# Performance work log

Measured on AMD Instinct MI355X. Metric: run time of the kernel, lower is better.

The kernel has to match this reference:

```python
import jax, jax.numpy as jnp
import numpy as np

NUM_CODES = 512
CODE_DIM = 64
COMMITMENT_COST = 0.25


def setup_inputs() -> dict:
    key = jax.random.key(0)
    k1, k2 = jax.random.split(key)
    latents = jax.random.normal(k1, (32, 4096, CODE_DIM), dtype=jnp.float32)
    # nn.Embedding weight init: uniform(-1/num_codes, 1/num_codes)
    codebook = jax.random.uniform(
        k2, (NUM_CODES, CODE_DIM), dtype=jnp.float32,
        minval=-1.0 / NUM_CODES, maxval=1.0 / NUM_CODES)
    return {"latents": latents, "codebook": codebook}


def reference(latents, codebook):
    shape = latents.shape
    flat = latents.reshape(-1, CODE_DIM)                      # [N, D]
    x2 = jnp.sum(flat * flat, axis=-1, keepdims=True)         # [N, 1]
    c2 = jnp.sum(codebook * codebook, axis=-1)                # [K]
    xc = flat @ codebook.T                                    # [N, K] dense GEMM
    dist2 = x2 - 2.0 * xc + c2[None, :]
    codes = jnp.argmin(dist2, axis=-1)                        # [N] int
    quantized = codebook[codes].reshape(shape)                # gather + reshape
    sg = jax.lax.stop_gradient
    commitment_loss = jnp.mean((latents - sg(quantized)) ** 2)
    embedding_loss = jnp.mean((quantized - sg(latents)) ** 2)
    vq_loss = embedding_loss + COMMITMENT_COST * commitment_loss
    quantized_st = latents + sg(quantized - latents)          # straight-through
    return quantized_st, codes.reshape(shape[:-1]), vq_loss
```

## Files before the change

### kernel.cpp

```cpp
#include <hip/hip_runtime.h>

#define NUM_CODES 512
#define CODE_DIM 64
#define N_ROWS (32 * 4096)
#define ROWS_PER_BLOCK 64
#define WAVES_PER_BLOCK 4
#define CODES_PER_WAVE (NUM_CODES / WAVES_PER_BLOCK)
#define KU 4

__global__ void vq_precompute_c2(const float* __restrict__ cb,
                                 float* __restrict__ c2) {
    int k = blockIdx.x * blockDim.x + threadIdx.x;
    if (k < NUM_CODES) {
        const float* c = cb + (size_t)k * CODE_DIM;
        float s = 0.f;
#pragma unroll
        for (int d = 0; d < CODE_DIM; ++d) s = fmaf(c[d], c[d], s);
        c2[k] = s;
    }
}

__global__ __launch_bounds__(256) void vq_main(
    const float* __restrict__ latents, const float* __restrict__ cb,
    const float* __restrict__ c2, float* __restrict__ out_q,
    float* __restrict__ out_codes, float* __restrict__ loss_accum) {
    const int lane = threadIdx.x & 63;
    const int wave = threadIdx.x >> 6;
    const int row = blockIdx.x * ROWS_PER_BLOCK + lane;
    const int chunk0 = __builtin_amdgcn_readfirstlane(wave) * CODES_PER_WAVE;

    const float* __restrict__ x = latents + (size_t)row * CODE_DIM;

    float xv[CODE_DIM];
#pragma unroll
    for (int i = 0; i < CODE_DIM / 4; ++i) {
        float4 v = reinterpret_cast<const float4*>(x)[i];
        xv[4 * i + 0] = v.x;
        xv[4 * i + 1] = v.y;
        xv[4 * i + 2] = v.z;
        xv[4 * i + 3] = v.w;
    }

    float x2 = 0.f;
#pragma unroll
    for (int d = 0; d < CODE_DIM; ++d) x2 = fmaf(xv[d], xv[d], x2);

    float bestd = __builtin_inff();
    int bk = 0;
    for (int kk = 0; kk < CODES_PER_WAVE; kk += KU) {
        const int k0 = chunk0 + kk;
        const float* __restrict__ c = cb + (size_t)k0 * CODE_DIM;
        float s0 = 0.f, s1 = 0.f, s2 = 0.f, s3 = 0.f;
#pragma unroll
        for (int d = 0; d < CODE_DIM; ++d) {
            s0 = fmaf(xv[d], c[d + 0 * CODE_DIM], s0);
            s1 = fmaf(xv[d], c[d + 1 * CODE_DIM], s1);
            s2 = fmaf(xv[d], c[d + 2 * CODE_DIM], s2);
            s3 = fmaf(xv[d], c[d + 3 * CODE_DIM], s3);
        }
        float d0 = (x2 - 2.0f * s0) + c2[k0 + 0];
        float d1 = (x2 - 2.0f * s1) + c2[k0 + 1];
        float d2 = (x2 - 2.0f * s2) + c2[k0 + 2];
        float d3 = (x2 - 2.0f * s3) + c2[k0 + 3];
        if (d0 < bestd) { bestd = d0; bk = k0 + 0; }
        if (d1 < bestd) { bestd = d1; bk = k0 + 1; }
        if (d2 < bestd) { bestd = d2; bk = k0 + 2; }
        if (d3 < bestd) { bestd = d3; bk = k0 + 3; }
    }

    __shared__ float sdist[WAVES_PER_BLOCK][ROWS_PER_BLOCK];
    __shared__ int sidx[WAVES_PER_BLOCK][ROWS_PER_BLOCK];
    sdist[wave][lane] = bestd;
    sidx[wave][lane] = bk;
    __syncthreads();
    if (wave != 0) return;

    float bd = sdist[0][lane];
    int bi = sidx[0][lane];
#pragma unroll
    for (int w = 1; w < WAVES_PER_BLOCK; ++w) {
        float d = sdist[w][lane];
        int i = sidx[w][lane];
        if (d < bd) { bd = d; bi = i; }
    }

    const float* __restrict__ q = cb + (size_t)bi * CODE_DIM;
    float4* oq = reinterpret_cast<float4*>(out_q + (size_t)row * CODE_DIM);
    float lsum = 0.f;
#pragma unroll
    for (int i = 0; i < CODE_DIM / 4; ++i) {
        float4 qq = reinterpret_cast<const float4*>(q)[i];
        float xx0 = xv[4 * i + 0], xx1 = xv[4 * i + 1];
        float xx2 = xv[4 * i + 2], xx3 = xv[4 * i + 3];
        float e0 = xx0 - qq.x, e1 = xx1 - qq.y, e2 = xx2 - qq.z, e3 = xx3 - qq.w;
        lsum = fmaf(e0, e0, lsum);
        lsum = fmaf(e1, e1, lsum);
        lsum = fmaf(e2, e2, lsum);
        lsum = fmaf(e3, e3, lsum);
        float4 ov;
        ov.x = xx0 + (qq.x - xx0);
        ov.y = xx1 + (qq.y - xx1);
        ov.z = xx2 + (qq.z - xx2);
        ov.w = xx3 + (qq.w - xx3);
        oq[i] = ov;
    }
    out_codes[row] = (float)bi;

#pragma unroll
    for (int off = 32; off > 0; off >>= 1) lsum += __shfl_down(lsum, off);
    if (lane == 0) atomicAdd(loss_accum, lsum);
}

__global__ void vq_finalize(const float* __restrict__ acc,
                            float* __restrict__ out_loss) {
    *out_loss = 1.25f * (*acc) / (float)(N_ROWS * CODE_DIM);
}

extern "C" void kernel_launch(void* const* d_in, const int* in_sizes, int n_in,
                              void* d_out, int out_size, void* d_ws, size_t ws_size,
                              hipStream_t stream) {
    const float* latents = (const float*)d_in[0];
    const float* cb      = (const float*)d_in[1];

    float* out_q     = (float*)d_out;
    float* out_codes = out_q + (size_t)N_ROWS * CODE_DIM;
    float* out_loss  = out_codes + N_ROWS;

    float* c2  = (float*)d_ws;
    float* acc = c2 + NUM_CODES;

    hipMemsetAsync(acc, 0, sizeof(float), stream);
    vq_precompute_c2<<<2, 256, 0, stream>>>(cb, c2);
    vq_main<<<N_ROWS / ROWS_PER_BLOCK, 256, 0, stream>>>(latents, cb, c2, out_q,
                                                         out_codes, acc);
    vq_finalize<<<1, 1, 0, stream>>>(acc, out_loss);
}
```

Before: 243.2 us.

## Load codebook rows via scalar SMEM loads and coalesce output epilogue across waves

The distance loop now loads each wave-uniform codebook row and its norm with inline-asm s_load_dwordx16 into SGPRs. This replaces per-lane vector loads of uniform data and lets the FMAs take scalar operands. The epilogue is restructured so all four waves write the quantized output row-by-row, one coalesced dword per lane, instead of wave 0 doing strided per-thread float4 stores. The loss is reduced in shared memory before a single atomic per block. The trade-offs are a full lgkmcnt(0) wait every code with no unrolling, which limits latency hiding, and the latents being re-read from global memory.

```diff
diff --git a/kernel.cpp b/kernel.cpp
--- a/kernel.cpp
+++ b/kernel.cpp
@@ -6,7 +6,15 @@
 #define ROWS_PER_BLOCK 64
 #define WAVES_PER_BLOCK 4
 #define CODES_PER_WAVE (NUM_CODES / WAVES_PER_BLOCK)
-#define KU 4
+
+typedef float f32x16 __attribute__((ext_vector_type(16)));
+
+static __device__ inline const float* uniform_ptr(const float* p) {
+    uint64_t u = (uint64_t)p;
+    uint32_t lo = __builtin_amdgcn_readfirstlane((uint32_t)u);
+    uint32_t hi = __builtin_amdgcn_readfirstlane((uint32_t)(u >> 32));
+    return (const float*)(((uint64_t)hi << 32) | lo);
+}
 
 __global__ void vq_precompute_c2(const float* __restrict__ cb,
                                  float* __restrict__ c2) {
@@ -20,17 +28,16 @@
     }
 }
 
-__global__ __launch_bounds__(256) void vq_main(
+__global__ __launch_bounds__(256, 4) void vq_main(
     const float* __restrict__ latents, const float* __restrict__ cb,
-    const float* __restrict__ c2, float* __restrict__ out_q,
+    const float* __restrict__ c2g, float* __restrict__ out_q,
     float* __restrict__ out_codes, float* __restrict__ loss_accum) {
     const int lane = threadIdx.x & 63;
     const int wave = threadIdx.x >> 6;
     const int row = blockIdx.x * ROWS_PER_BLOCK + lane;
-    const int chunk0 = __builtin_amdgcn_readfirstlane(wave) * CODES_PER_WAVE;
+    const int chunk0 = wave * CODES_PER_WAVE;
 
     const float* __restrict__ x = latents + (size_t)row * CODE_DIM;
-
     float xv[CODE_DIM];
 #pragma unroll
     for (int i = 0; i < CODE_DIM / 4; ++i) {
@@ -40,75 +47,82 @@
         xv[4 * i + 2] = v.z;
         xv[4 * i + 3] = v.w;
     }
-
     float x2 = 0.f;
 #pragma unroll
     for (int d = 0; d < CODE_DIM; ++d) x2 = fmaf(xv[d], xv[d], x2);
 
     float bestd = __builtin_inff();
     int bk = 0;
-    for (int kk = 0; kk < CODES_PER_WAVE; kk += KU) {
-        const int k0 = chunk0 + kk;
-        const float* __restrict__ c = cb + (size_t)k0 * CODE_DIM;
-        float s0 = 0.f, s1 = 0.f, s2 = 0.f, s3 = 0.f;
+    const float* cp = uniform_ptr(cb + (size_t)chunk0 * CODE_DIM);
+    const float* zp = uniform_ptr(c2g + chunk0);
+
+#pragma unroll 1
+    for (int k = 0; k < CODES_PER_WAVE; ++k) {
+        f32x16 c0, c1, c2, c3;
+        float zz;
+        asm volatile("s_load_dwordx16 %0, %1, 0x00" : "=s"(c0) : "s"(cp));
+        asm volatile("s_load_dwordx16 %0, %1, 0x40" : "=s"(c1) : "s"(cp));
+        asm volatile("s_load_dwordx16 %0, %1, 0x80" : "=s"(c2) : "s"(cp));
+        asm volatile("s_load_dwordx16 %0, %1, 0xc0" : "=s"(c3) : "s"(cp));
+        asm volatile("s_load_dword %0, %1, 0x00" : "=s"(zz) : "s"(zp));
+        asm volatile("s_waitcnt lgkmcnt(0)"
+                     : "+s"(c0), "+s"(c1), "+s"(c2), "+s"(c3), "+s"(zz));
+
+        float s = 0.f;
 #pragma unroll
-        for (int d = 0; d < CODE_DIM; ++d) {
-            s0 = fmaf(xv[d], c[d + 0 * CODE_DIM], s0);
-            s1 = fmaf(xv[d], c[d + 1 * CODE_DIM], s1);
-            s2 = fmaf(xv[d], c[d + 2 * CODE_DIM], s2);
-            s3 = fmaf(xv[d], c[d + 3 * CODE_DIM], s3);
-        }
-        float d0 = (x2 - 2.0f * s0) + c2[k0 + 0];
-        float d1 = (x2 - 2.0f * s1) + c2[k0 + 1];
-        float d2 = (x2 - 2.0f * s2) + c2[k0 + 2];
-        float d3 = (x2 - 2.0f * s3) + c2[k0 + 3];
-        if (d0 < bestd) { bestd = d0; bk = k0 + 0; }
-        if (d1 < bestd) { bestd = d1; bk = k0 + 1; }
-        if (d2 < bestd) { bestd = d2; bk = k0 + 2; }
-        if (d3 < bestd) { bestd = d3; bk = k0 + 3; }
+        for (int q = 0; q < 16; ++q) s = fmaf(xv[q], c0[q], s);
+#pragma unroll
+        for (int q = 0; q < 16; ++q) s = fmaf(xv[16 + q], c1[q], s);
+#pragma unroll
+        for (int q = 0; q < 16; ++q) s = fmaf(xv[32 + q], c2[q], s);
+#pragma unroll
+        for (int q = 0; q < 16; ++q) s = fmaf(xv[48 + q], c3[q], s);
+
+        float dist = (x2 - 2.0f * s) + zz;
+        if (dist < bestd) { bestd = dist; bk = chunk0 + k; }
+        cp += CODE_DIM;
+        zp += 1;
     }
 
     __shared__ float sdist[WAVES_PER_BLOCK][ROWS_PER_BLOCK];
     __shared__ int sidx[WAVES_PER_BLOCK][ROWS_PER_BLOCK];
+    __shared__ int sbi[ROWS_PER_BLOCK];
     sdist[wave][lane] = bestd;
     sidx[wave][lane] = bk;
     __syncthreads();
-    if (wave != 0) return;
+    if (wave == 0) {
+        float bd = sdist[0][lane];
+        int bi = sidx[0][lane];
+#pragma unroll
+        for (int w = 1; w < WAVES_PER_BLOCK; ++w) {
+            float d = sdist[w][lane];
+            int i = sidx[w][lane];
+            if (d < bd) { bd = d; bi = i; }
+        }
+        sbi[lane] = bi;
+    }
+    __syncthreads();
 
-    float bd = sdist[0][lane];
-    int bi = sidx[0][lane];
-#pragma unroll
-    for (int w = 1; w < WAVES_PER_BLOCK; ++w) {
-        float d = sdist[w][lane];
-        int i = sidx[w][lane];
-        if (d < bd) { bd = d; bi = i; }
-    }
-
-    const float* __restrict__ q = cb + (size_t)bi * CODE_DIM;
-    float4* oq = reinterpret_cast<float4*>(out_q + (size_t)row * CODE_DIM);
     float lsum = 0.f;
 #pragma unroll
-    for (int i = 0; i < CODE_DIM / 4; ++i) {
-        float4 qq = reinterpret_cast<const float4*>(q)[i];
-        float xx0 = xv[4 * i + 0], xx1 = xv[4 * i + 1];
-        float xx2 = xv[4 * i + 2], xx3 = xv[4 * i + 3];
-        float e0 = xx0 - qq.x, e1 = xx1 - qq.y, e2 = xx2 - qq.z, e3 = xx3 - qq.w;
-        lsum = fmaf(e0, e0, lsum);
-        lsum = fmaf(e1, e1, lsum);
-        lsum = fmaf(e2, e2, lsum);
-        lsum = fmaf(e3, e3, lsum);
-        float4 ov;
-        ov.x = xx0 + (qq.x - xx0);
-        ov.y = xx1 + (qq.y - xx1);
-        ov.z = xx2 + (qq.z - xx2);
-        ov.w = xx3 + (qq.w - xx3);
-        oq[i] = ov;
+    for (int rr = 0; rr < 16; ++rr) {
+        const int r = wave * 16 + rr;
+        const size_t grow = (size_t)blockIdx.x * ROWS_PER_BLOCK + r;
+        const int bi = sbi[r];
+        float xd = latents[grow * CODE_DIM + lane];
+        float qd = cb[(size_t)bi * CODE_DIM + lane];
+        float e = xd - qd;
+        lsum = fmaf(e, e, lsum);
+        out_q[grow * CODE_DIM + lane] = xd + (qd - xd);
+        if (lane == 0) out_codes[grow] = (float)bi;
     }
-    out_codes[row] = (float)bi;
-
 #pragma unroll
     for (int off = 32; off > 0; off >>= 1) lsum += __shfl_down(lsum, off);
-    if (lane == 0) atomicAdd(loss_accum, lsum);
+    __shared__ float red[WAVES_PER_BLOCK];
+    if (lane == 0) red[wave] = lsum;
+    __syncthreads();
+    if (threadIdx.x == 0)
+        atomicAdd(loss_accum, red[0] + red[1] + red[2] + red[3]);
 }
 
 __global__ void vq_finalize(const float* __restrict__ acc,
```

After: 227.5 us. 1.07x faster.
